# Kernel tuning notes

Measured on AMD Instinct MI355X. Metric: run time of the kernel, lower is better.

Reference implementation:

```python
import jax, jax.numpy as jnp
import numpy as np
from jax import lax

B, C, H, W, FS = 2, 3, 512, 512, 51


def setup_inputs() -> dict:
    key = jax.random.key(0)
    k1, k2, k3 = jax.random.split(key, 3)
    input1 = jax.random.normal(k1, (B, C, H + FS - 1, W + FS - 1), dtype=jnp.float32)
    input2 = jax.random.uniform(k2, (B, FS, H, W), dtype=jnp.float32)  # vertical kernels
    input3 = jax.random.uniform(k3, (B, FS, H, W), dtype=jnp.float32)  # horizontal kernels
    return {"input1": input1, "input2": input2, "input3": input3}


def _sepconv(input1, input2, input3):
    # out[b,c,y,x] = sum_{i,j} input1[b,c,y+i,x+j] * input2[b,i,y,x] * input3[b,j,y,x]
    fs = input2.shape[1]
    b, c, hp, wp = input1.shape
    h = hp - fs + 1
    w = wp - fs + 1

    def body(acc, i):
        # rows shifted by vertical offset i: [B,C,H,Wp]
        rows = lax.dynamic_slice_in_dim(input1, i, h, axis=2)
        # horizontal sliding windows of width fs: [B,C,H,W,fs]
        wins = jnp.stack([lax.slice_in_dim(rows, j, j + w, axis=3) for j in range(fs)], axis=-1)
        # adaptive horizontal filtering with per-pixel kernels
        hf = jnp.einsum('bchwj,bjhw->bchw', wins, input3)
        # weight by vertical kernel tap i and accumulate
        vi = lax.dynamic_index_in_dim(input2, i, axis=1, keepdims=False)  # [B,H,W]
        return acc + hf * vi[:, None, :, :], None

    acc0 = jnp.zeros((b, c, h, w), dtype=input1.dtype)
    out, _ = lax.scan(body, acc0, jnp.arange(fs))
    return out


def reference(input1, input2, input3):
    return _sepconv(input1, input2, input3)
```

## Files before the change

### kernel.cpp

```cpp
#include <hip/hip_runtime.h>
#include <cstdint>

namespace {

typedef _Float16 half2v __attribute__((ext_vector_type(2)));
typedef _Float16 half8 __attribute__((ext_vector_type(8)));
typedef float f32x4 __attribute__((ext_vector_type(4)));
typedef unsigned int u32x4 __attribute__((ext_vector_type(4)));

constexpr int KFS = 51;
constexpr int NB = 2, NC = 3, HH = 512, WW = 512;
constexpr int HP = HH + KFS - 1;
constexpr int WP = WW + KFS - 1;
constexpr size_t VSTR = (size_t)HH * WW;

constexpr int XCH = 32;
constexpr int YR = 8;
constexpr int NTHREADS = 512;
constexpr int NROWS = YR + 64 - 1;
constexpr int AFP = NROWS * 4;
constexpr int ASZ = NC * 3 * 4 * AFP;
constexpr int AV = NC * 3 * 4 * NROWS;
constexpr int SS = 26;
constexpr int SLSZ = YR * SS * 32;

__device__ __forceinline__ uint32_t pack2(float a, float b) {
  half2v p;
  p.x = (_Float16)a;
  p.y = (_Float16)b;
  return __builtin_bit_cast(uint32_t, p);
}

__global__ __launch_bounds__(NTHREADS, 4)
void sepconv_mfma(const float* __restrict__ in1, const float* __restrict__ in2,
                  const float* __restrict__ in3, float* __restrict__ out) {
  __shared__ __align__(16) uint32_t ALDS[ASZ];
  __shared__ uint32_t SLAB[SLSZ];

  const int t = threadIdx.x;
  const int lane = t & 63;
  const int w = t >> 6;
  const int l15 = lane & 15;
  const int lq = lane >> 4;

  const int x0 = blockIdx.x * XCH;
  const int y0 = blockIdx.y * YR;
  const int b = blockIdx.z;

  const float* in1b = in1 + (size_t)b * NC * HP * WP;
  const float* v2 = in2 + (size_t)b * KFS * VSTR;
  const float* h3 = in3 + (size_t)b * KFS * VSTR;
  const int y = y0 + w;

  float vw[4][2][4];
  #pragma unroll
  for (int mt = 0; mt < 4; ++mt)
    #pragma unroll
    for (int nt = 0; nt < 2; ++nt)
      #pragma unroll
      for (int r = 0; r < 4; ++r) {
        const int m = mt * 16 + lq * 4 + r;
        vw[mt][nt][r] = (m < KFS)
            ? v2[(size_t)m * VSTR + (size_t)y * WW + x0 + nt * 16 + l15] : 0.f;
      }

  {
    const int e2 = t & 3;
    int v = t >> 2;
    int ww = (v >= NROWS) ? 1 : 0;
    int r = v - ww * NROWS;
    #pragma unroll 1
    for (int s = 0; s < 20; ++s) {
      if (v < AV) {
        const int lqi = ww & 3;
        const int cks = ww >> 2;
        const int c = cks / 3;
        const int ks = cks - 3 * c;
        const int k0 = ks * 32 + lqi * 8 + 2 * e2;
        const int row = min(y0 + r, HP - 1);
        float2 g = make_float2(0.f, 0.f);
        if (k0 < 82)
          g = *reinterpret_cast<const float2*>(in1b + ((size_t)c * HP + row) * WP + x0 + k0);
        ALDS[(v << 2) | e2] = pack2(g.x, g.y);
      }
      v += 128;
      r += 57; ww += 1;
      if (r >= NROWS) { r -= NROWS; ww += 1; }
    }
  }
  {
    const int n = t & 31;
    int sidx = t >> 5;
    int yy = 0;
    #pragma unroll 1
    for (int s13 = 0; s13 < 13; ++s13) {
      const float* hp = h3 + (size_t)(y0 + yy) * WW + x0 + n;
      const float a = hp[(size_t)(2 * sidx) * VSTR];
      const float bq = (2 * sidx + 1 < KFS) ? hp[(size_t)(2 * sidx + 1) * VSTR] : 0.f;
      SLAB[(yy * SS + sidx) * 32 + n] = pack2(a, bq);
      sidx += 16;
      if (sidx >= SS) { sidx -= SS; ++yy; }
    }
  }
  __syncthreads();

  const uint32_t* SLy = &SLAB[w * SS * 32];
  const int sh = (l15 & 1) * 16;

  u32x4 bf[2][3];
  #pragma unroll
  for (int nt = 0; nt < 2; ++nt) {
    const int n = nt * 16 + l15;
    #pragma unroll
    for (int ks = 0; ks < 3; ++ks) {
      const int j0 = ks * 32 + lq * 8 - n;
      const int sB = j0 >> 1;
      uint32_t P[5];
      #pragma unroll
      for (int u = 0; u < 5; ++u) {
        const int s = sB + u;
        const int sc = min(max(s, 0), SS - 1);
        const uint32_t pv = SLy[sc * 32 + n];
        P[u] = ((unsigned)s <= (unsigned)(SS - 1)) ? pv : 0u;
      }
      u32x4 f;
      f.x = __builtin_amdgcn_alignbit(P[1], P[0], sh);
      f.y = __builtin_amdgcn_alignbit(P[2], P[1], sh);
      f.z = __builtin_amdgcn_alignbit(P[3], P[2], sh);
      f.w = __builtin_amdgcn_alignbit(P[4], P[3], sh);
      bf[nt][ks] = f;
    }
  }

  float ps[2][NC] = {};
  #pragma unroll
  for (int mt = 0; mt < 4; ++mt) {
    #pragma unroll
    for (int c = 0; c < NC; ++c) {
      u32x4 af[3];
      #pragma unroll
      for (int ks = 0; ks < 3; ++ks)
        af[ks] = *reinterpret_cast<const u32x4*>(
            &ALDS[((c * 3 + ks) * 4 + lq) * AFP + (w + mt * 16 + l15) * 4]);
      #pragma unroll
      for (int nt = 0; nt < 2; ++nt) {
        f32x4 acc = {0.f, 0.f, 0.f, 0.f};
        #pragma unroll
        for (int ks = 0; ks < 3; ++ks)
          acc = __builtin_amdgcn_mfma_f32_16x16x32_f16(
              __builtin_bit_cast(half8, af[ks]),
              __builtin_bit_cast(half8, bf[nt][ks]), acc, 0, 0, 0);
        float p = acc[0] * vw[mt][nt][0];
        p = fmaf(acc[1], vw[mt][nt][1], p);
        p = fmaf(acc[2], vw[mt][nt][2], p);
        p = fmaf(acc[3], vw[mt][nt][3], p);
        ps[nt][c] += p;
      }
    }
  }

  #pragma unroll
  for (int c = 0; c < NC; ++c) {
    float pa = ps[0][c];
    pa += __shfl_xor(pa, 16);
    pa += __shfl_xor(pa, 32);
    float pb = ps[1][c];
    pb += __shfl_xor(pb, 16);
    pb += __shfl_xor(pb, 32);
    const float po = (lane < 16) ? pa : pb;
    if (lane < 32)
      out[((size_t)(b * NC + c) * HH + y) * WW + x0 + lane] = po;
  }
}

}

extern "C" void kernel_launch(void* const* d_in, const int* in_sizes, int n_in,
                              void* d_out, int out_size, void* d_ws, size_t ws_size,
                              hipStream_t stream) {
  const float* in1 = (const float*)d_in[0];
  const float* in2 = (const float*)d_in[1];
  const float* in3 = (const float*)d_in[2];
  float* out = (float*)d_out;

  dim3 grid(WW / XCH, HH / YR, NB);
  sepconv_mfma<<<grid, NTHREADS, 0, stream>>>(in1, in2, in3, out);
}
```

Baseline: 80.22 us.

## Batch global loads into registers before LDS stores and pad horizontal slab

The staging loops are restructured so each wave loads its own row of horizontal kernel taps directly into registers up front. The input-tile loads are issued in unrolled batches of ten before their LDS stores, which puts more memory requests in flight. The horizontal slab gains a zero-padded entry at each end, so the boundary select in the B-fragment build becomes a single clamp into the padding. Register pressure rises (26 plus 20 floats held live), which may hurt occupancy at the 4-blocks launch bound.

```diff
diff --git a/kernel.cpp b/kernel.cpp
--- a/kernel.cpp
+++ b/kernel.cpp
@@ -22,7 +22,8 @@
 constexpr int ASZ = NC * 3 * 4 * AFP;
 constexpr int AV = NC * 3 * 4 * NROWS;
 constexpr int SS = 26;
-constexpr int SLSZ = YR * SS * 32;
+constexpr int SLROW = SS + 2;
+constexpr int SLSZ = YR * SLROW * 32;
 
 __device__ __forceinline__ uint32_t pack2(float a, float b) {
   half2v p;
@@ -64,49 +65,64 @@
             ? v2[(size_t)m * VSTR + (size_t)y * WW + x0 + nt * 16 + l15] : 0.f;
       }
 
+  uint32_t* SLW = &SLAB[w * SLROW * 32];
+  const int sn = lane & 31;
+  const int shf = lane >> 5;
+  float sa[13], sb[13];
   {
-    const int e2 = t & 3;
+    const float* hp = h3 + (size_t)y * WW + x0 + sn;
+    #pragma unroll
+    for (int i = 0; i < 13; ++i) {
+      const int s = 2 * i + shf;
+      sa[i] = hp[(size_t)(2 * s) * VSTR];
+      sb[i] = (2 * s + 1 < KFS) ? hp[(size_t)(2 * s + 1) * VSTR] : 0.f;
+    }
+  }
+
+  const int e2 = t & 3;
+  {
     int v = t >> 2;
-    int ww = (v >= NROWS) ? 1 : 0;
-    int r = v - ww * NROWS;
-    #pragma unroll 1
-    for (int s = 0; s < 20; ++s) {
-      if (v < AV) {
-        const int lqi = ww & 3;
-        const int cks = ww >> 2;
-        const int c = cks / 3;
-        const int ks = cks - 3 * c;
-        const int k0 = ks * 32 + lqi * 8 + 2 * e2;
-        const int row = min(y0 + r, HP - 1);
+    int ww2 = (v >= NROWS) ? 1 : 0;
+    int r = v - ww2 * NROWS;
+    float2 ga[10];
+    #pragma unroll
+    for (int half = 0; half < 2; ++half) {
+      #pragma unroll
+      for (int s = 0; s < 10; ++s) {
         float2 g = make_float2(0.f, 0.f);
-        if (k0 < 82)
-          g = *reinterpret_cast<const float2*>(in1b + ((size_t)c * HP + row) * WP + x0 + k0);
-        ALDS[(v << 2) | e2] = pack2(g.x, g.y);
-      }
-      v += 128;
-      r += 57; ww += 1;
-      if (r >= NROWS) { r -= NROWS; ww += 1; }
-    }
-  }
-  {
-    const int n = t & 31;
-    int sidx = t >> 5;
-    int yy = 0;
-    #pragma unroll 1
-    for (int s13 = 0; s13 < 13; ++s13) {
-      const float* hp = h3 + (size_t)(y0 + yy) * WW + x0 + n;
-      const float a = hp[(size_t)(2 * sidx) * VSTR];
-      const float bq = (2 * sidx + 1 < KFS) ? hp[(size_t)(2 * sidx + 1) * VSTR] : 0.f;
-      SLAB[(yy * SS + sidx) * 32 + n] = pack2(a, bq);
-      sidx += 16;
-      if (sidx >= SS) { sidx -= SS; ++yy; }
-    }
+        if (v < AV) {
+          const int lqi = ww2 & 3;
+          const int cks = ww2 >> 2;
+          const int c = cks / 3;
+          const int ks = cks - 3 * c;
+          const int k0 = ks * 32 + lqi * 8 + 2 * e2;
+          const int row = min(y0 + r, HP - 1);
+          if (k0 < 82)
+            g = *reinterpret_cast<const float2*>(
+                in1b + ((size_t)c * HP + row) * WP + x0 + k0);
+        }
+        ga[s] = g;
+        v += 128; r += 57; ww2 += 1;
+        if (r >= NROWS) { r -= NROWS; ++ww2; }
+      }
+      #pragma unroll
+      for (int s = 0; s < 10; ++s) {
+        const int vv = (t >> 2) + 128 * (half * 10 + s);
+        if (vv < AV) ALDS[(vv << 2) | e2] = pack2(ga[s].x, ga[s].y);
+      }
+    }
+  }
+
+  SLW[(shf ? (SLROW - 1) : 0) * 32 + sn] = 0u;
+  #pragma unroll
+  for (int i = 0; i < 13; ++i) {
+    const int s = 2 * i + shf;
+    SLW[(s + 1) * 32 + sn] = pack2(sa[i], sb[i]);
   }
   __syncthreads();
 
-  const uint32_t* SLy = &SLAB[w * SS * 32];
+  const uint32_t* SLy = SLW;
   const int sh = (l15 & 1) * 16;
-
   u32x4 bf[2][3];
   #pragma unroll
   for (int nt = 0; nt < 2; ++nt) {
@@ -118,10 +134,8 @@
       uint32_t P[5];
       #pragma unroll
       for (int u = 0; u < 5; ++u) {
-        const int s = sB + u;
-        const int sc = min(max(s, 0), SS - 1);
-        const uint32_t pv = SLy[sc * 32 + n];
-        P[u] = ((unsigned)s <= (unsigned)(SS - 1)) ? pv : 0u;
+        const int sc = min(max(sB + u, -1), SS) + 1;
+        P[u] = SLy[sc * 32 + n];
       }
       u32x4 f;
       f.x = __builtin_amdgcn_alignbit(P[1], P[0], sh);
```

After: 65.37 us. 18.5% less time.
